# Kernel tuning notes

Measured on AMD Instinct MI355X. Metric: run time of the kernel, lower is better.

The kernel has to match this reference:

```python
import jax, jax.numpy as jnp
import numpy as np

D_INNER, D_STATE, DT_RANK = 2048, 16, 128
BATCH, SEQ = 2, 2048


def setup_inputs() -> dict:
    key = jax.random.key(0)
    ks = jax.random.split(key, 6)
    x = jax.random.normal(ks[0], (BATCH, SEQ, D_INNER), dtype=jnp.float32)
    # A_log initialized uniform(-4, -1) per _init_parameters
    A_log = jax.random.uniform(ks[1], (D_INNER, D_STATE), minval=-4.0, maxval=-1.0, dtype=jnp.float32)
    D = jnp.ones((D_INNER,), dtype=jnp.float32)
    # torch Linear weights: [out_features, in_features], kaiming-uniform-ish scale
    x_proj_w = jax.random.normal(ks[2], (DT_RANK + 2 * D_STATE, D_INNER), dtype=jnp.float32) / np.sqrt(D_INNER)
    dt_proj_w = jax.random.normal(ks[3], (D_INNER, DT_RANK), dtype=jnp.float32) / np.sqrt(DT_RANK)
    dt_std = DT_RANK ** (-0.5)
    dt_proj_b = jax.random.uniform(ks[4], (D_INNER,), minval=-dt_std, maxval=dt_std, dtype=jnp.float32)
    return {"x": x, "A_log": A_log, "D": D, "x_proj_w": x_proj_w,
            "dt_proj_w": dt_proj_w, "dt_proj_b": dt_proj_b}


def _selective_scan(u, delta, A, B, C, D):
    # u, delta: [b, l, d]; A: [d, n]; B, C: [b, l, n]; D: [d]
    dA = jnp.exp(delta[..., None] * A[None, None])          # [b, l, d, n]
    dBu = (delta * u)[..., None] * B[:, :, None, :]         # [b, l, d, n]

    def step(h, inp):
        dA_t, dBu_t, C_t = inp                              # [b,d,n],[b,d,n],[b,n]
        h = dA_t * h + dBu_t
        y_t = jnp.einsum('bdn,bn->bd', h, C_t)
        return h, y_t

    h0 = jnp.zeros((u.shape[0], u.shape[2], A.shape[1]), dtype=u.dtype)
    xs = (jnp.moveaxis(dA, 1, 0), jnp.moveaxis(dBu, 1, 0), jnp.moveaxis(C, 1, 0))
    _, ys = jax.lax.scan(step, h0, xs)                      # ys: [l, b, d]
    y = jnp.moveaxis(ys, 0, 1)
    return y + u * D[None, None, :]


def reference(x, A_log, D, x_proj_w, dt_proj_w, dt_proj_b):
    # x: [b, l, d_inner]
    x_dbl = jnp.einsum('bld,ed->ble', x, x_proj_w)          # [b, l, dt_rank + 2n]
    delta_r = x_dbl[..., :DT_RANK]
    B = x_dbl[..., DT_RANK:DT_RANK + D_STATE]
    C = x_dbl[..., DT_RANK + D_STATE:]
    delta = jnp.einsum('blr,dr->bld', delta_r, dt_proj_w) + dt_proj_b
    delta = jax.nn.softplus(delta)                          # delta_softplus=True
    A = -jnp.exp(A_log)
    return _selective_scan(x, delta, A, B, C, D)
```

## Files before the change

### kernel.cpp

```cpp
#include <hip/hip_runtime.h>
#include <hip/hip_bf16.h>
#include <math.h>

#define DI   2048
#define DS   16
#define DTR  128
#define NBATCH 2
#define SEQ  2048
#define ROWS (NBATCH*SEQ)
#define NE   (DTR + 2*DS)
#define NC   32
#define LC   (SEQ/NC)
#define KS1  16

typedef float f32x4 __attribute__((ext_vector_type(4)));
typedef short s16x8 __attribute__((ext_vector_type(8)));
typedef short s16x4 __attribute__((ext_vector_type(4)));

__device__ inline short f2bf(float f) {
    unsigned u = __builtin_bit_cast(unsigned, f);
    u += 0x7FFFu + ((u >> 16) & 1u);
    return (short)(u >> 16);
}

__device__ inline unsigned pk2(float lo, float hi) {
    union { __hip_bfloat162 h; unsigned u; } cv;
    cv.h = __float22bfloat162_rn(float2{lo, hi});
    return cv.u;
}
__device__ inline unsigned packdu(short dbf, float xf) {
    return ((unsigned)(unsigned short)f2bf(xf) << 16) | (unsigned)(unsigned short)dbf;
}

__global__ __launch_bounds__(256) void k_castw(const float* __restrict__ w,
                                               const float* __restrict__ dtw,
                                               short* __restrict__ wb,
                                               short* __restrict__ dtwb) {
    int i = blockIdx.x*256 + threadIdx.x;
    if (i < 81920) {
        float4 v = ((const float4*)w)[i];
        s16x4 o = { f2bf(v.x), f2bf(v.y), f2bf(v.z), f2bf(v.w) };
        *(s16x4*)(wb + 4*i) = o;
    } else if (i < 147456) {
        int j = i - 81920;
        float4 v = ((const float4*)dtw)[j];
        s16x4 o = { f2bf(v.x), f2bf(v.y), f2bf(v.z), f2bf(v.w) };
        *(s16x4*)(dtwb + 4*j) = o;
    }
}

__global__ __launch_bounds__(256) void k_gemm1(const float* __restrict__ x,
                                               const short* __restrict__ wb,
                                               float* __restrict__ part) {
    const int wave = blockIdx.x*4 + (threadIdx.x >> 6);
    const int lane = threadIdx.x & 63;
    const int m16 = wave & 255;
    const int ks  = wave >> 8;
    const int r = lane & 15, g = lane >> 4;
    f32x4 acc[10];
    #pragma unroll
    for (int i = 0; i < 10; i++) acc[i] = (f32x4){0.f,0.f,0.f,0.f};

    const float* xp = x + (size_t)(m16*16 + r)*DI + g*8;
    #pragma unroll
    for (int kk = 0; kk < 4; ++kk) {
        const int k0 = ks*128 + kk*32;
        float4 xa = *(const float4*)(xp + k0);
        float4 xc = *(const float4*)(xp + k0 + 4);
        union { s16x8 v; unsigned u[4]; } af;
        af.u[0] = pk2(xa.x, xa.y);
        af.u[1] = pk2(xa.z, xa.w);
        af.u[2] = pk2(xc.x, xc.y);
        af.u[3] = pk2(xc.z, xc.w);
        const short* bp = wb + (size_t)r*DI + k0 + g*8;
        #pragma unroll
        for (int nf = 0; nf < 10; ++nf) {
            s16x8 bfrag = *(const s16x8*)(bp + (size_t)nf*16*DI);
            acc[nf] = __builtin_amdgcn_mfma_f32_16x16x32_bf16(af.v, bfrag, acc[nf], 0, 0, 0);
        }
    }
    const int orow = m16*16 + g*4;
    #pragma unroll
    for (int nf = 0; nf < 10; ++nf)
        #pragma unroll
        for (int j = 0; j < 4; ++j)
            part[((size_t)ks*ROWS + orow + j)*NE + nf*16 + r] = acc[nf][j];
}

__global__ __launch_bounds__(256) void k_split(const float* __restrict__ part,
                                               short* __restrict__ dRb,
                                               float* __restrict__ Bm,
                                               float* __restrict__ Cm) {
    int i = blockIdx.x*256 + threadIdx.x;
    if (i >= ROWS*NE) return;
    float v = 0.f;
    #pragma unroll
    for (int s = 0; s < KS1; ++s) v += part[(size_t)s*ROWS*NE + i];
    int row = i / NE, e = i - row*NE;
    if (e < DTR)            dRb[(size_t)row*DTR + e] = f2bf(v);
    else if (e < DTR + DS)  Bm[(size_t)row*DS + (e - DTR)] = v;
    else                    Cm[(size_t)row*DS + (e - DTR - DS)] = v;
}

__global__ __launch_bounds__(256) void k_gemm2(const short* __restrict__ dRb,
                                               const short* __restrict__ dtwb,
                                               const float* __restrict__ bias,
                                               unsigned short* __restrict__ deltab) {
    const int wave = blockIdx.x*4 + (threadIdx.x >> 6);
    const int lane = threadIdx.x & 63;
    const int m16 = wave >> 5, nt = wave & 31;
    const int r = lane & 15, g = lane >> 4;

    s16x8 a[4];
    const short* ap = dRb + (size_t)(m16*16 + r)*DTR + g*8;
    #pragma unroll
    for (int ks = 0; ks < 4; ++ks) a[ks] = *(const s16x8*)(ap + ks*32);

    f32x4 acc[4];
    #pragma unroll
    for (int i = 0; i < 4; i++) acc[i] = (f32x4){0.f,0.f,0.f,0.f};

    #pragma unroll
    for (int nf = 0; nf < 4; ++nf) {
        const short* bp = dtwb + (size_t)(nt*64 + nf*16 + r)*DTR + g*8;
        #pragma unroll
        for (int ks = 0; ks < 4; ++ks) {
            s16x8 b = *(const s16x8*)(bp + ks*32);
            acc[nf] = __builtin_amdgcn_mfma_f32_16x16x32_bf16(a[ks], b, acc[nf], 0, 0, 0);
        }
    }
    const int orow = m16*16 + g*4;
    #pragma unroll
    for (int nf = 0; nf < 4; ++nf) {
        const int col = nt*64 + nf*16 + r;
        const float bb = bias[col];
        #pragma unroll
        for (int j = 0; j < 4; ++j) {
            float v = acc[nf][j] + bb;
            float sp = fmaxf(v, 0.f) + __logf(1.f + __expf(-fabsf(v)));
            deltab[(size_t)(orow + j)*DI + col] = (unsigned short)f2bf(sp);
        }
    }
}

__global__ __launch_bounds__(256) void k_scan1(const unsigned short* __restrict__ deltab,
                                               const float* __restrict__ x,
                                               const float* __restrict__ Bm,
                                               const float* __restrict__ A_log,
                                               float* __restrict__ aprod,
                                               float* __restrict__ rsum) {
    __shared__ unsigned lxd[LC][64];
    __shared__ float lB[LC][DS];
    const int tid = threadIdx.x;
    const int bb = blockIdx.x & 31;
    const int b  = (blockIdx.x >> 5) & 1;
    const int c  = blockIdx.x >> 6;
    const int d0 = bb*64;
    const int lbase = c*LC;

    {
        const unsigned short* dsrc = deltab + ((size_t)(b*SEQ + lbase))*DI + d0;
        const float*          xsrc = x      + ((size_t)(b*SEQ + lbase))*DI + d0;
        const int row = tid >> 4, col = (tid & 15)*4;
        #pragma unroll
        for (int i = 0; i < 4; i++) {
            s16x4  dv = *(const s16x4*) (dsrc + (size_t)(row + 16*i)*DI + col);
            float4 xv = *(const float4*)(xsrc + (size_t)(row + 16*i)*DI + col);
            uint4 o;
            o.x = packdu(dv[0], xv.x);
            o.y = packdu(dv[1], xv.y);
            o.z = packdu(dv[2], xv.z);
            o.w = packdu(dv[3], xv.w);
            *(uint4*)&lxd[row + 16*i][col] = o;
        }
        const float* bsrc = Bm + ((size_t)(b*SEQ + lbase))*DS;
        *(float4*)&lB[tid >> 2][(tid & 3)*4] = *(const float4*)(bsrc + tid*4);
    }

    const int lane = tid & 63, widx = tid >> 6;
    const int dlow = lane & 15, q = lane >> 4;
    const int dcol = widx*16 + dlow;
    const int d = d0 + dcol;
    const int n0 = 4*q;

    float4 Alg = *(const float4*)(A_log + (size_t)d*DS + n0);
    float An[4] = { -__expf(Alg.x), -__expf(Alg.y), -__expf(Alg.z), -__expf(Alg.w) };
    float ap[4] = {1.f,1.f,1.f,1.f}, r[4] = {0.f,0.f,0.f,0.f};

    __syncthreads();

    #pragma unroll 8
    for (int tt = 0; tt < LC; ++tt) {
        unsigned v = lxd[tt][dcol];
        float dlt = __builtin_bit_cast(float, v << 16);
        float u   = __builtin_bit_cast(float, v & 0xffff0000u);
        float du  = dlt * u;
        float4 bv = *(const float4*)&lB[tt][n0];
        float bbv[4] = {bv.x, bv.y, bv.z, bv.w};
        #pragma unroll
        for (int j = 0; j < 4; ++j) {
            float da = __expf(dlt * An[j]);
            r[j]  = fmaf(da, r[j], du * bbv[j]);
            ap[j] *= da;
        }
    }
    size_t base = (((size_t)c*NBATCH + b)*DI + d)*DS + n0;
    *(float4*)(aprod + base) = (float4){ap[0], ap[1], ap[2], ap[3]};
    *(float4*)(rsum  + base) = (float4){r[0],  r[1],  r[2],  r[3]};
}

__global__ __launch_bounds__(256) void k_mid(const float* __restrict__ aprod,
                                             const float* __restrict__ rsum,
                                             float* __restrict__ hin) {
    int gid = blockIdx.x*256 + threadIdx.x;
    int n = gid & 15;
    int d = (gid >> 4) & (DI-1);
    int b = gid >> 15;
    float h = 0.f;
    for (int c = 0; c < NC; c++) {
        size_t idx = (((size_t)c*NBATCH + b)*DI + d)*DS + n;
        hin[idx] = h;
        h = fmaf(aprod[idx], h, rsum[idx]);
    }
}

__global__ __launch_bounds__(256) void k_scan2(const unsigned short* __restrict__ deltab,
                                               const float* __restrict__ x,
                                               const float* __restrict__ Bm,
                                               const float* __restrict__ Cm,
                                               const float* __restrict__ A_log,
                                               const float* __restrict__ Dv,
                                               const float* __restrict__ hin,
                                               float* __restrict__ y) {
    __shared__ unsigned lxd[LC][64];
    __shared__ float lB[LC][DS];
    __shared__ float lC[LC][DS];
    const int tid = threadIdx.x;
    const int bb = blockIdx.x & 31;
    const int b  = (blockIdx.x >> 5) & 1;
    const int c  = blockIdx.x >> 6;
    const int d0 = bb*64;
    const int lbase = c*LC;

    {
        const unsigned short* dsrc = deltab + ((size_t)(b*SEQ + lbase))*DI + d0;
        const float*          xsrc = x      + ((size_t)(b*SEQ + lbase))*DI + d0;
        const int row = tid >> 4, col = (tid & 15)*4;
        #pragma unroll
        for (int i = 0; i < 4; i++) {
            s16x4  dv = *(const s16x4*) (dsrc + (size_t)(row + 16*i)*DI + col);
            float4 xv = *(const float4*)(xsrc + (size_t)(row + 16*i)*DI + col);
            uint4 o;
            o.x = packdu(dv[0], xv.x);
            o.y = packdu(dv[1], xv.y);
            o.z = packdu(dv[2], xv.z);
            o.w = packdu(dv[3], xv.w);
            *(uint4*)&lxd[row + 16*i][col] = o;
        }
        const float* bsrc = Bm + ((size_t)(b*SEQ + lbase))*DS;
        const float* csrc = Cm + ((size_t)(b*SEQ + lbase))*DS;
        *(float4*)&lB[tid >> 2][(tid & 3)*4] = *(const float4*)(bsrc + tid*4);
        *(float4*)&lC[tid >> 2][(tid & 3)*4] = *(const float4*)(csrc + tid*4);
    }

    const int lane = tid & 63, widx = tid >> 6;
    const int dlow = lane & 15, q = lane >> 4;
    const int dcol = widx*16 + dlow;
    const int d = d0 + dcol;
    const int n0 = 4*q;

    float4 Alg = *(const float4*)(A_log + (size_t)d*DS + n0);
    float An[4] = { -__expf(Alg.x), -__expf(Alg.y), -__expf(Alg.z), -__expf(Alg.w) };
    size_t base = (((size_t)c*NBATCH + b)*DI + d)*DS + n0;
    float4 hv = *(const float4*)(hin + base);
    float h[4] = {hv.x, hv.y, hv.z, hv.w};
    const float Dd = Dv[d];
    float* yp = y + ((size_t)(b*SEQ + lbase))*DI + d;

    __syncthreads();

    #pragma unroll 8
    for (int tt = 0; tt < LC; ++tt) {
        unsigned v = lxd[tt][dcol];
        float dlt = __builtin_bit_cast(float, v << 16);
        float u   = __builtin_bit_cast(float, v & 0xffff0000u);
        float du  = dlt * u;
        float4 bv = *(const float4*)&lB[tt][n0];
        float4 cv = *(const float4*)&lC[tt][n0];
        float bbv[4] = {bv.x, bv.y, bv.z, bv.w};
        float ccv[4] = {cv.x, cv.y, cv.z, cv.w};
        float acc = 0.f;
        #pragma unroll
        for (int j = 0; j < 4; ++j) {
            float da = __expf(dlt * An[j]);
            h[j] = fmaf(da, h[j], du * bbv[j]);
            acc  = fmaf(h[j], ccv[j], acc);
        }
        acc += __shfl_xor(acc, 16);
        acc += __shfl_xor(acc, 32);
        if (q == 0) yp[(size_t)tt*DI] = fmaf(u, Dd, acc);
    }
}

extern "C" void kernel_launch(void* const* d_in, const int* in_sizes, int n_in,
                              void* d_out, int out_size, void* d_ws, size_t ws_size,
                              hipStream_t stream) {
    const float* x     = (const float*)d_in[0];
    const float* A_log = (const float*)d_in[1];
    const float* Dv    = (const float*)d_in[2];
    const float* xpw   = (const float*)d_in[3];
    const float* dtw   = (const float*)d_in[4];
    const float* dtb   = (const float*)d_in[5];
    float* out = (float*)d_out;

    const size_t SCN = (size_t)NC*NBATCH*DS*DI;
    const size_t PARTN = (size_t)KS1*ROWS*NE;

    float* ws    = (float*)d_ws;
    unsigned short* deltab = (unsigned short*)ws;
    float* unionR= ws + ((size_t)ROWS*DI/2);
    float* part  = unionR;
    float* aprod = unionR;
    float* rsum  = aprod + SCN;
    float* hin   = rsum  + SCN;
    float* uend  = unionR + ((3*SCN > PARTN) ? 3*SCN : PARTN);
    float* Bm    = uend;
    float* Cm    = Bm + (size_t)ROWS*DS;
    short* dRb   = (short*)(Cm + (size_t)ROWS*DS);
    short* wb    = dRb + (size_t)ROWS*DTR;
    short* dtwb  = wb  + (size_t)160*2048;

    k_castw<<<576, 256, 0, stream>>>(xpw, dtw, wb, dtwb);
    k_gemm1<<<1024, 256, 0, stream>>>(x, wb, part);
    k_split<<<(ROWS*NE + 255)/256, 256, 0, stream>>>(part, dRb, Bm, Cm);
    k_gemm2<<<2048, 256, 0, stream>>>(dRb, dtwb, dtb, deltab);
    k_scan1<<<2048, 256, 0, stream>>>(deltab, x, Bm, A_log, aprod, rsum);
    k_mid<<<256, 256, 0, stream>>>(aprod, rsum, hin);
    k_scan2<<<2048, 256, 0, stream>>>(deltab, x, Bm, Cm, A_log, Dv, hin, out);
}
```

Baseline: 214.0 us.

## Drop split-K in projection GEMM, double scan chunks, compute chunk decay from delta sum

The first projection GEMM no longer splits K into 16 partial buffers followed by a reduction kernel. Each wave now covers the full K range for half of the output columns and writes dRb/B/C directly, which removes the k_split kernel and its partial-sum traffic but launches only 128 blocks. The scan chunk count doubles to 64, giving twice as many scan blocks of half the length. The per-chunk decay product is now computed as exp(A*sum(delta)) instead of a running product, and k_mid writes the carried state in place over the decay buffer.

```diff
diff --git a/kernel.cpp b/kernel.cpp
--- a/kernel.cpp
+++ b/kernel.cpp
@@ -9,9 +9,8 @@
 #define SEQ  2048
 #define ROWS (NBATCH*SEQ)
 #define NE   (DTR + 2*DS)
-#define NC   32
+#define NC   64
 #define LC   (SEQ/NC)
-#define KS1  16
 
 typedef float f32x4 __attribute__((ext_vector_type(4)));
 typedef short s16x8 __attribute__((ext_vector_type(8)));
@@ -51,20 +50,23 @@
 
 __global__ __launch_bounds__(256) void k_gemm1(const float* __restrict__ x,
                                                const short* __restrict__ wb,
-                                               float* __restrict__ part) {
+                                               short* __restrict__ dRb,
+                                               float* __restrict__ Bm,
+                                               float* __restrict__ Cm) {
     const int wave = blockIdx.x*4 + (threadIdx.x >> 6);
     const int lane = threadIdx.x & 63;
-    const int m16 = wave & 255;
-    const int ks  = wave >> 8;
+    const int m16  = wave & 255;
+    const int half = wave >> 8;
     const int r = lane & 15, g = lane >> 4;
-    f32x4 acc[10];
-    #pragma unroll
-    for (int i = 0; i < 10; i++) acc[i] = (f32x4){0.f,0.f,0.f,0.f};
+    f32x4 acc[5];
+    #pragma unroll
+    for (int i = 0; i < 5; i++) acc[i] = (f32x4){0.f,0.f,0.f,0.f};
 
     const float* xp = x + (size_t)(m16*16 + r)*DI + g*8;
-    #pragma unroll
-    for (int kk = 0; kk < 4; ++kk) {
-        const int k0 = ks*128 + kk*32;
+    const short* wbase = wb + (size_t)(half*80 + r)*DI + g*8;
+    #pragma unroll 2
+    for (int kk = 0; kk < 64; ++kk) {
+        const int k0 = kk*32;
         float4 xa = *(const float4*)(xp + k0);
         float4 xc = *(const float4*)(xp + k0 + 4);
         union { s16x8 v; unsigned u[4]; } af;
@@ -72,34 +74,26 @@
         af.u[1] = pk2(xa.z, xa.w);
         af.u[2] = pk2(xc.x, xc.y);
         af.u[3] = pk2(xc.z, xc.w);
-        const short* bp = wb + (size_t)r*DI + k0 + g*8;
-        #pragma unroll
-        for (int nf = 0; nf < 10; ++nf) {
-            s16x8 bfrag = *(const s16x8*)(bp + (size_t)nf*16*DI);
+        #pragma unroll
+        for (int nf = 0; nf < 5; ++nf) {
+            s16x8 bfrag = *(const s16x8*)(wbase + (size_t)nf*16*DI + k0);
             acc[nf] = __builtin_amdgcn_mfma_f32_16x16x32_bf16(af.v, bfrag, acc[nf], 0, 0, 0);
         }
     }
     const int orow = m16*16 + g*4;
     #pragma unroll
-    for (int nf = 0; nf < 10; ++nf)
-        #pragma unroll
-        for (int j = 0; j < 4; ++j)
-            part[((size_t)ks*ROWS + orow + j)*NE + nf*16 + r] = acc[nf][j];
-}
-
-__global__ __launch_bounds__(256) void k_split(const float* __restrict__ part,
-                                               short* __restrict__ dRb,
-                                               float* __restrict__ Bm,
-                                               float* __restrict__ Cm) {
-    int i = blockIdx.x*256 + threadIdx.x;
-    if (i >= ROWS*NE) return;
-    float v = 0.f;
-    #pragma unroll
-    for (int s = 0; s < KS1; ++s) v += part[(size_t)s*ROWS*NE + i];
-    int row = i / NE, e = i - row*NE;
-    if (e < DTR)            dRb[(size_t)row*DTR + e] = f2bf(v);
-    else if (e < DTR + DS)  Bm[(size_t)row*DS + (e - DTR)] = v;
-    else                    Cm[(size_t)row*DS + (e - DTR - DS)] = v;
+    for (int nf = 0; nf < 5; ++nf) {
+        const int gnf = half*5 + nf;
+        const int col = gnf*16 + r;
+        #pragma unroll
+        for (int j = 0; j < 4; ++j) {
+            const int row = orow + j;
+            float v = acc[nf][j];
+            if (gnf < 8)       dRb[(size_t)row*DTR + col]        = f2bf(v);
+            else if (gnf == 8) Bm [(size_t)row*DS + (col - 128)] = v;
+            else               Cm [(size_t)row*DS + (col - 144)] = v;
+        }
+    }
 }
 
 __global__ __launch_bounds__(256) void k_gemm2(const short* __restrict__ dRb,
@@ -163,7 +157,7 @@
         const float*          xsrc = x      + ((size_t)(b*SEQ + lbase))*DI + d0;
         const int row = tid >> 4, col = (tid & 15)*4;
         #pragma unroll
-        for (int i = 0; i < 4; i++) {
+        for (int i = 0; i < 2; i++) {
             s16x4  dv = *(const s16x4*) (dsrc + (size_t)(row + 16*i)*DI + col);
             float4 xv = *(const float4*)(xsrc + (size_t)(row + 16*i)*DI + col);
             uint4 o;
@@ -173,8 +167,10 @@
             o.w = packdu(dv[3], xv.w);
             *(uint4*)&lxd[row + 16*i][col] = o;
         }
-        const float* bsrc = Bm + ((size_t)(b*SEQ + lbase))*DS;
-        *(float4*)&lB[tid >> 2][(tid & 3)*4] = *(const float4*)(bsrc + tid*4);
+        if (tid < 128) {
+            const float* bsrc = Bm + ((size_t)(b*SEQ + lbase))*DS;
+            *(float4*)&lB[tid >> 2][(tid & 3)*4] = *(const float4*)(bsrc + tid*4);
+        }
     }
 
     const int lane = tid & 63, widx = tid >> 6;
@@ -185,7 +181,8 @@
 
     float4 Alg = *(const float4*)(A_log + (size_t)d*DS + n0);
     float An[4] = { -__expf(Alg.x), -__expf(Alg.y), -__expf(Alg.z), -__expf(Alg.w) };
-    float ap[4] = {1.f,1.f,1.f,1.f}, r[4] = {0.f,0.f,0.f,0.f};
+    float r[4] = {0.f,0.f,0.f,0.f};
+    float S = 0.f;
 
     __syncthreads();
 
@@ -195,23 +192,23 @@
         float dlt = __builtin_bit_cast(float, v << 16);
         float u   = __builtin_bit_cast(float, v & 0xffff0000u);
         float du  = dlt * u;
+        S += dlt;
         float4 bv = *(const float4*)&lB[tt][n0];
         float bbv[4] = {bv.x, bv.y, bv.z, bv.w};
         #pragma unroll
         for (int j = 0; j < 4; ++j) {
             float da = __expf(dlt * An[j]);
-            r[j]  = fmaf(da, r[j], du * bbv[j]);
-            ap[j] *= da;
+            r[j] = fmaf(da, r[j], du * bbv[j]);
         }
     }
     size_t base = (((size_t)c*NBATCH + b)*DI + d)*DS + n0;
-    *(float4*)(aprod + base) = (float4){ap[0], ap[1], ap[2], ap[3]};
-    *(float4*)(rsum  + base) = (float4){r[0],  r[1],  r[2],  r[3]};
-}
-
-__global__ __launch_bounds__(256) void k_mid(const float* __restrict__ aprod,
-                                             const float* __restrict__ rsum,
-                                             float* __restrict__ hin) {
+    *(float4*)(aprod + base) = (float4){ __expf(An[0]*S), __expf(An[1]*S),
+                                         __expf(An[2]*S), __expf(An[3]*S) };
+    *(float4*)(rsum  + base) = (float4){ r[0], r[1], r[2], r[3] };
+}
+
+__global__ __launch_bounds__(256) void k_mid(float* ah,
+                                             const float* __restrict__ rsum) {
     int gid = blockIdx.x*256 + threadIdx.x;
     int n = gid & 15;
     int d = (gid >> 4) & (DI-1);
@@ -219,8 +216,10 @@
     float h = 0.f;
     for (int c = 0; c < NC; c++) {
         size_t idx = (((size_t)c*NBATCH + b)*DI + d)*DS + n;
-        hin[idx] = h;
-        h = fmaf(aprod[idx], h, rsum[idx]);
+        float a  = ah[idx];
+        float rr = rsum[idx];
+        ah[idx] = h;
+        h = fmaf(a, h, rr);
     }
 }
 
@@ -247,7 +246,7 @@
         const float*          xsrc = x      + ((size_t)(b*SEQ + lbase))*DI + d0;
         const int row = tid >> 4, col = (tid & 15)*4;
         #pragma unroll
-        for (int i = 0; i < 4; i++) {
+        for (int i = 0; i < 2; i++) {
             s16x4  dv = *(const s16x4*) (dsrc + (size_t)(row + 16*i)*DI + col);
             float4 xv = *(const float4*)(xsrc + (size_t)(row + 16*i)*DI + col);
             uint4 o;
@@ -257,10 +256,12 @@
             o.w = packdu(dv[3], xv.w);
             *(uint4*)&lxd[row + 16*i][col] = o;
         }
-        const float* bsrc = Bm + ((size_t)(b*SEQ + lbase))*DS;
-        const float* csrc = Cm + ((size_t)(b*SEQ + lbase))*DS;
-        *(float4*)&lB[tid >> 2][(tid & 3)*4] = *(const float4*)(bsrc + tid*4);
-        *(float4*)&lC[tid >> 2][(tid & 3)*4] = *(const float4*)(csrc + tid*4);
+        if (tid < 128) {
+            const float* bsrc = Bm + ((size_t)(b*SEQ + lbase))*DS;
+            const float* csrc = Cm + ((size_t)(b*SEQ + lbase))*DS;
+            *(float4*)&lB[tid >> 2][(tid & 3)*4] = *(const float4*)(bsrc + tid*4);
+            *(float4*)&lC[tid >> 2][(tid & 3)*4] = *(const float4*)(csrc + tid*4);
+        }
     }
 
     const int lane = tid & 63, widx = tid >> 6;
@@ -314,27 +315,21 @@
     float* out = (float*)d_out;
 
     const size_t SCN = (size_t)NC*NBATCH*DS*DI;
-    const size_t PARTN = (size_t)KS1*ROWS*NE;
 
     float* ws    = (float*)d_ws;
     unsigned short* deltab = (unsigned short*)ws;
-    float* unionR= ws + ((size_t)ROWS*DI/2);
-    float* part  = unionR;
-    float* aprod = unionR;
+    float* aprod = ws + ((size_t)ROWS*DI/2);
     float* rsum  = aprod + SCN;
-    float* hin   = rsum  + SCN;
-    float* uend  = unionR + ((3*SCN > PARTN) ? 3*SCN : PARTN);
-    float* Bm    = uend;
+    float* Bm    = rsum + SCN;
     float* Cm    = Bm + (size_t)ROWS*DS;
     short* dRb   = (short*)(Cm + (size_t)ROWS*DS);
     short* wb    = dRb + (size_t)ROWS*DTR;
     short* dtwb  = wb  + (size_t)160*2048;
 
     k_castw<<<576, 256, 0, stream>>>(xpw, dtw, wb, dtwb);
-    k_gemm1<<<1024, 256, 0, stream>>>(x, wb, part);
-    k_split<<<(ROWS*NE + 255)/256, 256, 0, stream>>>(part, dRb, Bm, Cm);
+    k_gemm1<<<128, 256, 0, stream>>>(x, wb, dRb, Bm, Cm);
     k_gemm2<<<2048, 256, 0, stream>>>(dRb, dtwb, dtb, deltab);
-    k_scan1<<<2048, 256, 0, stream>>>(deltab, x, Bm, A_log, aprod, rsum);
-    k_mid<<<256, 256, 0, stream>>>(aprod, rsum, hin);
-    k_scan2<<<2048, 256, 0, stream>>>(deltab, x, Bm, Cm, A_log, Dv, hin, out);
-}
+    k_scan1<<<4096, 256, 0, stream>>>(deltab, x, Bm, A_log, aprod, rsum);
+    k_mid<<<256, 256, 0, stream>>>(aprod, rsum);
+    k_scan2<<<4096, 256, 0, stream>>>(deltab, x, Bm, Cm, A_log, Dv, aprod, out);
+}
```

After: 228.5 us. 6.8% more time.
